# Optimization experiments

Measured on AMD Instinct MI355X. Metric: run time of the kernel, lower is better.

## Reference

```python
import jax, jax.numpy as jnp
import numpy as np

N, C, K, PARTS = 32, 256, 8192, 16
MAX_INIT = -100.0  # matches torch new_full((n,c,P), -100.0) with include_self=True


def setup_inputs() -> dict:
    key = jax.random.key(0)
    k1, k2, k3 = jax.random.split(key, 3)
    feats = jax.random.normal(k1, (N, C, K), dtype=jnp.float32)
    part_labels = jax.random.randint(k2, (K,), 0, PARTS, dtype=jnp.int64)
    valid_mask = jax.random.bernoulli(k3, 0.5, (N, K))
    return {"feats": feats, "part_labels": part_labels, "valid_mask": valid_mask}


def reference(feats, part_labels, valid_mask):
    n, c, k = feats.shape
    labels = part_labels.astype(jnp.int32)  # [k]
    vm = valid_mask.astype(feats.dtype)     # [n, k]

    # masked features for the mean branch (max branch uses raw feats, as in torch)
    valid_feat = feats * vm[:, None, :]      # [n, c, k]

    # scatter-add sum of valid features per part: [n, c, P]
    pooled_sum = jnp.zeros((n, c, PARTS), feats.dtype).at[:, :, labels].add(valid_feat)
    # scatter-add count of valid anchors per part: [n, P]
    pooled_count = jnp.zeros((n, PARTS), feats.dtype).at[:, labels].add(vm)
    # scatter-max over raw feats (unmasked, include_self with -100 init): [n, c, P]
    pooled_max = jnp.full((n, c, PARTS), MAX_INIT, feats.dtype).at[:, :, labels].max(feats)
    # anchors per part, independent of sample/mask: [P]
    patch_count = jnp.zeros((PARTS,), feats.dtype).at[labels].add(1.0)

    pooled_mean = pooled_sum / jnp.maximum(pooled_count, 1.0)[:, None, :]
    pooled_max = jnp.where(patch_count > 0, pooled_max, jnp.zeros_like(pooled_max))
    return pooled_mean + pooled_max  # [n, c, P]
```

## Files before the change

kernel.cpp:

```cpp
#include <hip/hip_runtime.h>

#define NN 32
#define CC 256
#define KK 8192
#define PARTS 16
#define TPB 256
#define PSTR 640
#define CH 16
#define NCH (CC / CH)
#define MAX_INIT (-100.0f)

typedef unsigned int uint32;
typedef unsigned short u16;

__device__ __forceinline__ uint32 swz(uint32 g) {
    return g ^ (((g >> 3) ^ (g >> 6)) & 7u);
}


__global__ __launch_bounds__(TPB) void sortA(const int* __restrict__ labels,
                                             int* __restrict__ pcount,
                                             u16* __restrict__ permbase) {
    __shared__ u16 lh[PARTS * TPB];
    __shared__ u16 pexc[PARTS * TPB];
    __shared__ u16 wtot[PARTS][4];
    __shared__ u16 s_hist[PARTS];
    __shared__ __align__(16) u16 s_perm[PARTS * PSTR];
    const int t = threadIdx.x;
    const int w = t >> 6;
    const int lane = t & 63;

#pragma unroll
    for (int p = 0; p < PARTS; ++p) lh[p * TPB + t] = 0;
    int4 lv[8];
    const int4* l4 = (const int4*)labels + t * 8;
#pragma unroll
    for (int i = 0; i < 8; ++i) lv[i] = l4[i];
    __syncthreads();

#pragma unroll
    for (int i = 0; i < 8; ++i) {
        int la[4] = {lv[i].x, lv[i].y, lv[i].z, lv[i].w};
#pragma unroll
        for (int j = 0; j < 4; ++j) lh[(la[j] & 15) * TPB + t]++;
    }
    __syncthreads();

    for (int p = 0; p < PARTS; ++p) {
        uint32 v = lh[p * TPB + t];
        uint32 inc = v;
#pragma unroll
        for (int s = 1; s < 64; s <<= 1) {
            uint32 o = __shfl_up(inc, s, 64);
            if (lane >= s) inc += o;
        }
        pexc[p * TPB + t] = (u16)(inc - v);
        if (lane == 63) wtot[p][w] = (u16)inc;
    }
    __syncthreads();
    for (int p = 0; p < PARTS; ++p) {
        uint32 base = 0;
        for (int ww = 0; ww < w; ++ww) base += wtot[p][ww];
        pexc[p * TPB + t] = (u16)(pexc[p * TPB + t] + base);
    }
    __syncthreads();
    if (t < PARTS) s_hist[t] = (u16)(pexc[t * TPB + TPB - 1] + lh[t * TPB + TPB - 1]);
    __syncthreads();

#pragma unroll
    for (int p = 0; p < PARTS; ++p) lh[p * TPB + t] = 0;
#pragma unroll
    for (int i = 0; i < 8; ++i) {
        int la[4] = {lv[i].x, lv[i].y, lv[i].z, lv[i].w};
#pragma unroll
        for (int j = 0; j < 4; ++j) {
            int k = t * 32 + i * 4 + j;
            int p = la[j] & 15;
            u16 c = lh[p * TPB + t];
            uint32 q = (uint32)pexc[p * TPB + t] + c;
            lh[p * TPB + t] = (u16)(c + 1);
            if (q < PSTR) s_perm[p * PSTR + q] = (u16)k;
        }
    }
    __syncthreads();

    {
        const int p = t >> 4;
        const int idx = t & 15;
        uint32 beg = s_hist[p];
        u16 fill = (u16)((beg ? (s_perm[p * PSTR] & 0x1fffu) : 0u) | 0x4000u);
        for (uint32 q = beg + idx; q < PSTR; q += 16) s_perm[p * PSTR + q] = fill;
        if (t < PARTS) pcount[t] = (int)s_hist[t];
    }
    __syncthreads();

    const uint4* src = (const uint4*)s_perm;
    uint4* dst = (uint4*)permbase;
#pragma unroll
    for (int j = 0; j < 5; ++j) dst[j * TPB + t] = src[j * TPB + t];
}

__global__ __launch_bounds__(TPB, 2) void pool_kernel(const float* __restrict__ feats,
                                                      const u16* __restrict__ permbase,
                                                      const int* __restrict__ pcount,
                                                      const int* __restrict__ vm,
                                                      float* __restrict__ out) {
    __shared__ uint32 srow[2 * KK];
    const int t = threadIdx.x;
    const int blk = blockIdx.x;
    const int n = blk / NCH;
    const int c0 = (blk % NCH) * CH;
    const int w = t >> 6;
    const int lane = t & 63;
    const int g = t >> 4;
    const int l = t & 15;

    {
        const int4* vmn4 = (const int4*)(vm + (size_t)n * KK) + t * 8;
        uint32 bits = 0;
#pragma unroll
        for (int j = 0; j < 8; ++j) {
            int4 v = vmn4[j];
            bits |= (uint32)(v.x != 0) << (4 * j) | (uint32)(v.y != 0) << (4 * j + 1) |
                    (uint32)(v.z != 0) << (4 * j + 2) | (uint32)(v.w != 0) << (4 * j + 3);
        }
        srow[t] = bits;
    }

    uint32 pk[20];
    {
        const uint4* pb4 = (const uint4*)(permbase + g * PSTR + l * 40);
#pragma unroll
        for (int j = 0; j < 5; ++j) {
            uint4 q = pb4[j];
            pk[j * 4 + 0] = q.x;
            pk[j * 4 + 1] = q.y;
            pk[j * 4 + 2] = q.z;
            pk[j * 4 + 3] = q.w;
        }
    }

    uint32 woff[8];
#pragma unroll
    for (int i = 0; i < 8; ++i) {
        uint32 r = (uint32)(w * 8 + i) * 64u + (uint32)lane;
        woff[i] = swz(r) * 4u;
    }
    __syncthreads();

    uint32 ga[40];
    float gm[40];
    int cnt = 0;
#pragma unroll
    for (int i = 0; i < 40; ++i) {
        uint32 e = (pk[i >> 1] >> (16 * (i & 1))) & 0xffffu;
        uint32 k = e & 0x1fffu;
        uint32 valid = (e & 0x4000u) ? 0u : ((srow[k >> 5] >> (k & 31u)) & 1u);
        uint32 pos = swz(k >> 2);
        ga[i] = pos * 16u + (k & 3u) * 4u;
        gm[i] = valid ? 1.0f : 0.0f;
        cnt += (int)valid;
    }
#pragma unroll
    for (int m = 1; m < 16; m <<= 1) cnt += __shfl_xor(cnt, m, 16);
    const float cv = fmaxf((float)cnt, 1.0f);
    const int ph = pcount[g];
    __syncthreads();

    auto STAGE = [&](int buf, int r) {
        const uint32* frow = (const uint32*)(feats + (size_t)(n * CC + c0 + r) * KK);
#pragma unroll
        for (int i = 0; i < 8; ++i) {
            __builtin_amdgcn_global_load_lds(
                (const __attribute__((address_space(1))) unsigned int*)(frow + woff[i]),
                (__attribute__((address_space(3))) unsigned int*)&srow[buf * KK + (w * 8 + i) * 256],
                16, 0, 0);
        }
    };

    STAGE(0, 0);
    for (int r = 0; r < CH; ++r) {
        const int cur = r & 1;
        const bool more = (r + 1 < CH);
        if (more) {
            STAGE(cur ^ 1, r + 1);
            asm volatile("s_waitcnt vmcnt(8)" ::: "memory");
        } else {
            asm volatile("s_waitcnt vmcnt(0)" ::: "memory");
        }
        __builtin_amdgcn_s_barrier();

        const char* rowb = (const char*)&srow[cur * KK];
        float rs0 = 0.0f, rs1 = 0.0f, rs2 = 0.0f, rs3 = 0.0f;
        float rm0 = MAX_INIT, rm1 = MAX_INIT, rm2 = MAX_INIT, rm3 = MAX_INIT;
#pragma unroll
        for (int i = 0; i < 40; i += 4) {
            float f0 = *(const float*)(rowb + ga[i]);
            float f1 = *(const float*)(rowb + ga[i + 1]);
            float f2 = *(const float*)(rowb + ga[i + 2]);
            float f3 = *(const float*)(rowb + ga[i + 3]);
            rm0 = fmaxf(rm0, f0);
            rs0 = fmaf(f0, gm[i], rs0);
            rm1 = fmaxf(rm1, f1);
            rs1 = fmaf(f1, gm[i + 1], rs1);
            rm2 = fmaxf(rm2, f2);
            rs2 = fmaf(f2, gm[i + 2], rs2);
            rm3 = fmaxf(rm3, f3);
            rs3 = fmaf(f3, gm[i + 3], rs3);
        }
        float rs = (rs0 + rs1) + (rs2 + rs3);
        float rm = fmaxf(fmaxf(rm0, rm1), fmaxf(rm2, rm3));
#pragma unroll
        for (int m = 1; m < 16; m <<= 1) {
            rs += __shfl_xor(rs, m, 16);
            rm = fmaxf(rm, __shfl_xor(rm, m, 16));
        }
        if (l == 0)
            out[(size_t)(n * CC + c0 + r) * PARTS + g] = rs / cv + (ph > 0 ? rm : 0.0f);

        if (more) __builtin_amdgcn_s_barrier();
    }
}

extern "C" void kernel_launch(void* const* d_in, const int* in_sizes, int n_in,
                              void* d_out, int out_size, void* d_ws, size_t ws_size,
                              hipStream_t stream) {
    const float* feats  = (const float*)d_in[0];
    const int*   labels = (const int*)d_in[1];
    const int*   vm     = (const int*)d_in[2];
    float* out = (float*)d_out;

    int* pcount   = (int*)d_ws;
    u16* permbase = (u16*)((char*)d_ws + 64);

    sortA<<<1, TPB, 0, stream>>>(labels, pcount, permbase);
    pool_kernel<<<NN * NCH, TPB, 0, stream>>>(feats, permbase, pcount, vm, out);
}
```

Before: 65.04 us.

## Parallelize prep across parts, precompute mask bits, prefetch two feature rows early

The single-block sort kernel becomes a 48-block prep kernel. Each of 16 blocks builds the permutation for one part, and 32 extra blocks pack the per-sample valid mask into bitmasks in the workspace. The pool kernel now reads the packed mask into a separate small shared array. It also issues the first two feature-row async loads before doing its index setup, so that setup overlaps with memory traffic, and it prefetches row r+2 after each row is consumed. The goal is to cut the serial prep latency and the pool kernel's startup stall, in exchange for an extra workspace buffer and slightly more LDS.

```diff
diff --git a/kernel.cpp b/kernel.cpp
--- a/kernel.cpp
+++ b/kernel.cpp
@@ -18,94 +18,90 @@
 }
 
 
-__global__ __launch_bounds__(TPB) void sortA(const int* __restrict__ labels,
-                                             int* __restrict__ pcount,
-                                             u16* __restrict__ permbase) {
-    __shared__ u16 lh[PARTS * TPB];
-    __shared__ u16 pexc[PARTS * TPB];
-    __shared__ u16 wtot[PARTS][4];
-    __shared__ u16 s_hist[PARTS];
-    __shared__ __align__(16) u16 s_perm[PARTS * PSTR];
+__global__ __launch_bounds__(TPB) void prep_kernel(const int* __restrict__ labels,
+                                                   const int* __restrict__ vm,
+                                                   int* __restrict__ pcount,
+                                                   u16* __restrict__ permbase,
+                                                   uint32* __restrict__ bmask) {
     const int t = threadIdx.x;
+    const int blk = blockIdx.x;
+
+    if (blk >= PARTS) {
+        const int n = blk - PARTS;
+        const int4* v4 = (const int4*)(vm + (size_t)n * KK) + t * 8;
+        uint32 bits = 0;
+#pragma unroll
+        for (int j = 0; j < 8; ++j) {
+            int4 v = v4[j];
+            bits |= (uint32)(v.x != 0) << (4 * j) | (uint32)(v.y != 0) << (4 * j + 1) |
+                    (uint32)(v.z != 0) << (4 * j + 2) | (uint32)(v.w != 0) << (4 * j + 3);
+        }
+        bmask[n * 256 + t] = bits;
+        return;
+    }
+
+    const int p = blk;
+    __shared__ __align__(16) u16 sperm[PSTR];
+    __shared__ u16 wtot[4];
+    __shared__ uint32 stot;
     const int w = t >> 6;
     const int lane = t & 63;
 
-#pragma unroll
-    for (int p = 0; p < PARTS; ++p) lh[p * TPB + t] = 0;
     int4 lv[8];
     const int4* l4 = (const int4*)labels + t * 8;
 #pragma unroll
-    for (int i = 0; i < 8; ++i) lv[i] = l4[i];
-    __syncthreads();
-
-#pragma unroll
-    for (int i = 0; i < 8; ++i) {
-        int la[4] = {lv[i].x, lv[i].y, lv[i].z, lv[i].w};
-#pragma unroll
-        for (int j = 0; j < 4; ++j) lh[(la[j] & 15) * TPB + t]++;
-    }
-    __syncthreads();
-
-    for (int p = 0; p < PARTS; ++p) {
-        uint32 v = lh[p * TPB + t];
-        uint32 inc = v;
-#pragma unroll
-        for (int s = 1; s < 64; s <<= 1) {
-            uint32 o = __shfl_up(inc, s, 64);
-            if (lane >= s) inc += o;
-        }
-        pexc[p * TPB + t] = (u16)(inc - v);
-        if (lane == 63) wtot[p][w] = (u16)inc;
-    }
-    __syncthreads();
-    for (int p = 0; p < PARTS; ++p) {
-        uint32 base = 0;
-        for (int ww = 0; ww < w; ++ww) base += wtot[p][ww];
-        pexc[p * TPB + t] = (u16)(pexc[p * TPB + t] + base);
-    }
-    __syncthreads();
-    if (t < PARTS) s_hist[t] = (u16)(pexc[t * TPB + TPB - 1] + lh[t * TPB + TPB - 1]);
-    __syncthreads();
-
-#pragma unroll
-    for (int p = 0; p < PARTS; ++p) lh[p * TPB + t] = 0;
-#pragma unroll
-    for (int i = 0; i < 8; ++i) {
-        int la[4] = {lv[i].x, lv[i].y, lv[i].z, lv[i].w};
-#pragma unroll
-        for (int j = 0; j < 4; ++j) {
-            int k = t * 32 + i * 4 + j;
-            int p = la[j] & 15;
-            u16 c = lh[p * TPB + t];
-            uint32 q = (uint32)pexc[p * TPB + t] + c;
-            lh[p * TPB + t] = (u16)(c + 1);
-            if (q < PSTR) s_perm[p * PSTR + q] = (u16)k;
-        }
-    }
-    __syncthreads();
-
-    {
-        const int p = t >> 4;
-        const int idx = t & 15;
-        uint32 beg = s_hist[p];
-        u16 fill = (u16)((beg ? (s_perm[p * PSTR] & 0x1fffu) : 0u) | 0x4000u);
-        for (uint32 q = beg + idx; q < PSTR; q += 16) s_perm[p * PSTR + q] = fill;
-        if (t < PARTS) pcount[t] = (int)s_hist[t];
-    }
-    __syncthreads();
-
-    const uint4* src = (const uint4*)s_perm;
-    uint4* dst = (uint4*)permbase;
-#pragma unroll
-    for (int j = 0; j < 5; ++j) dst[j * TPB + t] = src[j * TPB + t];
+    for (int j = 0; j < 8; ++j) lv[j] = l4[j];
+
+    uint32 c = 0;
+#pragma unroll
+    for (int j = 0; j < 8; ++j) {
+        c += ((lv[j].x & 15) == p) + ((lv[j].y & 15) == p) +
+             ((lv[j].z & 15) == p) + ((lv[j].w & 15) == p);
+    }
+    uint32 inc = c;
+#pragma unroll
+    for (int s = 1; s < 64; s <<= 1) {
+        uint32 o = __shfl_up(inc, s, 64);
+        if (lane >= s) inc += o;
+    }
+    if (lane == 63) wtot[w] = (u16)inc;
+    __syncthreads();
+    uint32 base = inc - c;
+    for (int ww = 0; ww < w; ++ww) base += wtot[ww];
+    if (t == TPB - 1) stot = base + c;
+
+    uint32 pos = base;
+#pragma unroll
+    for (int j = 0; j < 8; ++j) {
+        int la[4] = {lv[j].x, lv[j].y, lv[j].z, lv[j].w};
+#pragma unroll
+        for (int cc = 0; cc < 4; ++cc) {
+            if ((la[cc] & 15) == p) {
+                if (pos < PSTR) sperm[pos] = (u16)(t * 32 + j * 4 + cc);
+                ++pos;
+            }
+        }
+    }
+    __syncthreads();
+
+    const uint32 total = stot;
+    const u16 fill = (u16)((total ? (sperm[0] & 0x1fffu) : 0u) | 0x4000u);
+    for (uint32 q = total + t; q < PSTR; q += TPB) sperm[q] = fill;
+    if (t == 0) pcount[p] = (int)total;
+    __syncthreads();
+
+    const uint4* src = (const uint4*)sperm;
+    uint4* dst = (uint4*)(permbase + p * PSTR);
+    for (int i = t; i < PSTR * 2 / 16; i += TPB) dst[i] = src[i];
 }
 
 __global__ __launch_bounds__(TPB, 2) void pool_kernel(const float* __restrict__ feats,
                                                       const u16* __restrict__ permbase,
                                                       const int* __restrict__ pcount,
-                                                      const int* __restrict__ vm,
+                                                      const uint32* __restrict__ bmask,
                                                       float* __restrict__ out) {
     __shared__ uint32 srow[2 * KK];
+    __shared__ uint32 smask[256];
     const int t = threadIdx.x;
     const int blk = blockIdx.x;
     const int n = blk / NCH;
@@ -115,17 +111,28 @@
     const int g = t >> 4;
     const int l = t & 15;
 
-    {
-        const int4* vmn4 = (const int4*)(vm + (size_t)n * KK) + t * 8;
-        uint32 bits = 0;
-#pragma unroll
-        for (int j = 0; j < 8; ++j) {
-            int4 v = vmn4[j];
-            bits |= (uint32)(v.x != 0) << (4 * j) | (uint32)(v.y != 0) << (4 * j + 1) |
-                    (uint32)(v.z != 0) << (4 * j + 2) | (uint32)(v.w != 0) << (4 * j + 3);
-        }
-        srow[t] = bits;
-    }
+    uint32 woff[8];
+#pragma unroll
+    for (int i = 0; i < 8; ++i) {
+        uint32 r = (uint32)(w * 8 + i) * 64u + (uint32)lane;
+        woff[i] = swz(r) * 4u;
+    }
+
+    auto STAGE = [&](int buf, int r) {
+        const uint32* frow = (const uint32*)(feats + (size_t)(n * CC + c0 + r) * KK);
+#pragma unroll
+        for (int i = 0; i < 8; ++i) {
+            __builtin_amdgcn_global_load_lds(
+                (const __attribute__((address_space(1))) unsigned int*)(frow + woff[i]),
+                (__attribute__((address_space(3))) unsigned int*)&srow[buf * KK + (w * 8 + i) * 256],
+                16, 0, 0);
+        }
+    };
+
+    STAGE(0, 0);
+    STAGE(1, 1);
+
+    smask[t] = bmask[n * 256 + t];
 
     uint32 pk[20];
     {
@@ -139,13 +146,6 @@
             pk[j * 4 + 3] = q.w;
         }
     }
-
-    uint32 woff[8];
-#pragma unroll
-    for (int i = 0; i < 8; ++i) {
-        uint32 r = (uint32)(w * 8 + i) * 64u + (uint32)lane;
-        woff[i] = swz(r) * 4u;
-    }
     __syncthreads();
 
     uint32 ga[40];
@@ -155,7 +155,7 @@
     for (int i = 0; i < 40; ++i) {
         uint32 e = (pk[i >> 1] >> (16 * (i & 1))) & 0xffffu;
         uint32 k = e & 0x1fffu;
-        uint32 valid = (e & 0x4000u) ? 0u : ((srow[k >> 5] >> (k & 31u)) & 1u);
+        uint32 valid = (e & 0x4000u) ? 0u : ((smask[k >> 5] >> (k & 31u)) & 1u);
         uint32 pos = swz(k >> 2);
         ga[i] = pos * 16u + (k & 3u) * 4u;
         gm[i] = valid ? 1.0f : 0.0f;
@@ -165,32 +165,16 @@
     for (int m = 1; m < 16; m <<= 1) cnt += __shfl_xor(cnt, m, 16);
     const float cv = fmaxf((float)cnt, 1.0f);
     const int ph = pcount[g];
-    __syncthreads();
-
-    auto STAGE = [&](int buf, int r) {
-        const uint32* frow = (const uint32*)(feats + (size_t)(n * CC + c0 + r) * KK);
-#pragma unroll
-        for (int i = 0; i < 8; ++i) {
-            __builtin_amdgcn_global_load_lds(
-                (const __attribute__((address_space(1))) unsigned int*)(frow + woff[i]),
-                (__attribute__((address_space(3))) unsigned int*)&srow[buf * KK + (w * 8 + i) * 256],
-                16, 0, 0);
-        }
-    };
-
-    STAGE(0, 0);
+
     for (int r = 0; r < CH; ++r) {
-        const int cur = r & 1;
-        const bool more = (r + 1 < CH);
-        if (more) {
-            STAGE(cur ^ 1, r + 1);
+        if (r < CH - 1) {
             asm volatile("s_waitcnt vmcnt(8)" ::: "memory");
         } else {
             asm volatile("s_waitcnt vmcnt(0)" ::: "memory");
         }
         __builtin_amdgcn_s_barrier();
 
-        const char* rowb = (const char*)&srow[cur * KK];
+        const char* rowb = (const char*)&srow[(r & 1) * KK];
         float rs0 = 0.0f, rs1 = 0.0f, rs2 = 0.0f, rs3 = 0.0f;
         float rm0 = MAX_INIT, rm1 = MAX_INIT, rm2 = MAX_INIT, rm3 = MAX_INIT;
 #pragma unroll
@@ -218,7 +202,8 @@
         if (l == 0)
             out[(size_t)(n * CC + c0 + r) * PARTS + g] = rs / cv + (ph > 0 ? rm : 0.0f);
 
-        if (more) __builtin_amdgcn_s_barrier();
+        __builtin_amdgcn_s_barrier();
+        if (r + 2 < CH) STAGE(r & 1, r + 2);
     }
 }
 
@@ -230,9 +215,10 @@
     const int*   vm     = (const int*)d_in[2];
     float* out = (float*)d_out;
 
-    int* pcount   = (int*)d_ws;
-    u16* permbase = (u16*)((char*)d_ws + 64);
-
-    sortA<<<1, TPB, 0, stream>>>(labels, pcount, permbase);
-    pool_kernel<<<NN * NCH, TPB, 0, stream>>>(feats, permbase, pcount, vm, out);
-}
+    int*    pcount   = (int*)d_ws;
+    u16*    permbase = (u16*)((char*)d_ws + 64);
+    uint32* bmask    = (uint32*)((char*)d_ws + 24576);
+
+    prep_kernel<<<PARTS + NN, TPB, 0, stream>>>(labels, vm, pcount, permbase, bmask);
+    pool_kernel<<<NN * NCH, TPB, 0, stream>>>(feats, permbase, pcount, bmask, out);
+}
```

New measurement: 54.95 us, median of 3. 15.5% less time.
